# Optimization experiments

Measured on AMD Instinct MI355X. Metric: run time of the kernel, lower is better.

The kernel has to match this reference:

```python
import jax, jax.numpy as jnp
import numpy as np

K_SIZE = 7
D_MODEL = 128
D_Q = 64
N_HEADS = 4
D_FF = 512
EPS = 1e-5


def _windows(x, k):
    # x: [N,E,H,W] -> [N,E,P,H,W]; zero-padded local k x k windows,
    # row-major over (dy,dx), matching nn.Unfold ordering.
    p = k // 2
    N, E, H, W = x.shape
    xp = jnp.pad(x, ((0, 0), (0, 0), (p, p), (p, p)))
    ws = [xp[:, :, i:i + H, j:j + W] for i in range(k) for j in range(k)]
    return jnp.stack(ws, axis=2)


def _layernorm(x, g, b):
    m = jnp.mean(x, -1, keepdims=True)
    v = jnp.var(x, -1, keepdims=True)
    return (x - m) * jax.lax.rsqrt(v + EPS) * g + b


def setup_inputs() -> dict:
    key = jax.random.key(0)
    ks = jax.random.split(key, 12)
    E, Q, F = D_MODEL, D_Q, D_FF

    def g(k, shape, s=0.02):
        return jax.random.normal(k, shape, jnp.float32) * s

    return dict(
        x=jax.random.normal(ks[0], (4, E, 64, 64), jnp.float32),
        qcoeff=jax.random.normal(ks[1], (4, Q), jnp.float32),
        wq=g(ks[2], (E, E)), bq=jnp.zeros((E,), jnp.float32),
        wk=g(ks[3], (E, E)), bk=jnp.zeros((E,), jnp.float32),
        wv=g(ks[4], (E, E)), bv=jnp.zeros((E,), jnp.float32),
        rel_bias=jnp.zeros((N_HEADS, K_SIZE * K_SIZE), jnp.float32),
        ln1_g=jnp.ones((E,), jnp.float32), ln1_b=jnp.zeros((E,), jnp.float32),
        bil_w=g(ks[5], (E, E, Q)), bil_b=jnp.zeros((E,), jnp.float32),
        ln2_g=jnp.ones((E,), jnp.float32), ln2_b=jnp.zeros((E,), jnp.float32),
        w1=g(ks[6], (F, E)), b1=jnp.zeros((F,), jnp.float32),
        w2=g(ks[7], (E, F)), b2=jnp.zeros((E,), jnp.float32),
    )


def reference(x, qcoeff, wq, bq, wk, bk, wv, bv, rel_bias, ln1_g, ln1_b,
              bil_w, bil_b, ln2_g, ln2_b, w1, b1, w2, b2):
    N, E, H, W = x.shape
    Nh = N_HEADS
    Hd = E // Nh
    P = K_SIZE * K_SIZE

    x_nhwc = jnp.transpose(x, (0, 2, 3, 1))              # [N,H,W,E]
    xn = _layernorm(x_nhwc, ln1_g, ln1_b)
    xnc = jnp.transpose(xn, (0, 3, 1, 2))                # [N,E,H,W]

    # 1x1-conv projections
    q = jnp.einsum('nchw,oc->nohw', xnc, wq) + bq[None, :, None, None]
    k = jnp.einsum('nchw,oc->nohw', xnc, wk) + bk[None, :, None, None]
    v = jnp.einsum('nchw,oc->nohw', xnc, wv) + bv[None, :, None, None]

    # local windows of K/V: [N,Nh,Hd,P,H,W]
    Kw = _windows(k, K_SIZE).reshape(N, Nh, Hd, P, H, W)
    Vw = _windows(v, K_SIZE).reshape(N, Nh, Hd, P, H, W)
    Qh = q.reshape(N, Nh, Hd, H, W)

    scores = jnp.einsum('nhdyx,nhdpyx->nhpyx', Qh, Kw)
    scores = scores + rel_bias[None, :, :, None, None]
    attn = jax.nn.softmax(scores, axis=2)                # softmax over P
    out = jnp.einsum('nhpyx,nhdpyx->nhdyx', attn, Vw).reshape(N, E, H, W)
    z0 = jnp.transpose(out, (0, 2, 3, 1))                # [N,H,W,E]

    # Bilinear(z0, qcoeff): qcoeff constant per (H,W) -> contract once per batch
    t = jnp.einsum('oiq,nq->noi', bil_w, qcoeff)         # [N,E,E]
    z1 = jnp.einsum('nhwi,noi->nhwo', z0, t) + bil_b

    z2 = z1 + x_nhwc
    z3 = _layernorm(z2, ln2_g, ln2_b)
    h1 = jax.nn.gelu(z3 @ w1.T + b1, approximate=False)  # dropout inactive (eval)
    z4 = h1 @ w2.T + b2 + z2
    return jnp.transpose(z4, (0, 3, 1, 2))               # [N,E,H,W]
```

## Files before the change

### kernel.cpp

```cpp
#include <hip/hip_runtime.h>
#include <cmath>

#define EPS 1e-5f
#define SZ 2097152

typedef __attribute__((ext_vector_type(8))) short short8;
typedef __attribute__((ext_vector_type(4))) float floatx4;

__device__ __forceinline__ float dot4(float4 a, float4 b) {
  return fmaf(a.x, b.x, fmaf(a.y, b.y, fmaf(a.z, b.z, a.w * b.w)));
}

__device__ __forceinline__ short f2bf(float f) {
  union { float f; unsigned u; } v; v.f = f;
  unsigned r = v.u + 0x7fff + ((v.u >> 16) & 1);
  return (short)(r >> 16);
}

#define MFMA16(a, b, c) __builtin_amdgcn_mfma_f32_16x16x32_bf16(a, b, c, 0, 0, 0)

__global__ __launch_bounds__(256) void k_prep(const float* __restrict__ w1,
    const float* __restrict__ w2, const float* __restrict__ wq,
    const float* __restrict__ wk, const float* __restrict__ wv,
    const float* __restrict__ bil_w, const float* __restrict__ qcoeff,
    short* __restrict__ w1bf, short* __restrict__ w2bf,
    short* __restrict__ wqbf, short* __restrict__ wkbf, short* __restrict__ wvbf,
    short* __restrict__ tb) {
  __shared__ float qs[256];
  int tid = threadIdx.x;
  qs[tid] = qcoeff[tid];
  __syncthreads();
  int tid0 = blockIdx.x * 256 + tid;
  int stride = gridDim.x * 256;
  for (int i = tid0; i < 16384; i += stride) {
    int flat = i * 4; int f = flat >> 7, c = flat & 127;
    float4 v = *(const float4*)&w1[flat];
    short t4[4] = {f2bf(v.x), f2bf(v.y), f2bf(v.z), f2bf(v.w)};
    *(uint2*)&w1bf[f * 136 + c] = *(uint2*)t4;
  }
  for (int i = tid0; i < 16384; i += stride) {
    int flat = i * 4; int o = flat >> 9, j = flat & 511;
    int ck = j >> 7, jj = j & 127;
    float4 v = *(const float4*)&w2[flat];
    short t4[4] = {f2bf(v.x), f2bf(v.y), f2bf(v.z), f2bf(v.w)};
    *(uint2*)&w2bf[(ck * 128 + o) * 136 + jj] = *(uint2*)t4;
  }
  for (int i = tid0; i < 4096; i += stride) {
    int flat = i * 4; int o = flat >> 7, c = flat & 127;
    float4 a = *(const float4*)&wq[flat];
    float4 b = *(const float4*)&wk[flat];
    float4 cc = *(const float4*)&wv[flat];
    short ta[4] = {f2bf(a.x), f2bf(a.y), f2bf(a.z), f2bf(a.w)};
    short tb4[4] = {f2bf(b.x), f2bf(b.y), f2bf(b.z), f2bf(b.w)};
    short tc[4] = {f2bf(cc.x), f2bf(cc.y), f2bf(cc.z), f2bf(cc.w)};
    *(uint2*)&wqbf[o * 136 + c] = *(uint2*)ta;
    *(uint2*)&wkbf[o * 136 + c] = *(uint2*)tb4;
    *(uint2*)&wvbf[o * 136 + c] = *(uint2*)tc;
  }
  {
    int flat = tid0;
    const float* wrow = bil_w + (size_t)flat * 64;
    float acc[4] = {0.f, 0.f, 0.f, 0.f};
    for (int qq = 0; qq < 64; qq += 4) {
      float4 w4 = *(const float4*)&wrow[qq];
#pragma unroll
      for (int nn = 0; nn < 4; ++nn) {
        const float* qc = &qs[nn * 64 + qq];
        acc[nn] = fmaf(w4.x, qc[0], fmaf(w4.y, qc[1], fmaf(w4.z, qc[2], fmaf(w4.w, qc[3], acc[nn]))));
      }
    }
    int o = flat >> 7, i = flat & 127;
#pragma unroll
    for (int nn = 0; nn < 4; ++nn) tb[nn * 17408 + o * 136 + i] = f2bf(acc[nn]);
  }
}

__global__ __launch_bounds__(512) void k_qkvln(const float* __restrict__ x,
    const float* __restrict__ g, const float* __restrict__ b,
    const short* __restrict__ wqbf, const short* __restrict__ wkbf,
    const short* __restrict__ wvbf, const float* __restrict__ bq,
    const float* __restrict__ bk, const float* __restrict__ bv,
    float* __restrict__ xnhwc, short* __restrict__ qbf,
    short* __restrict__ kbf, short* __restrict__ vtb) {
  __shared__ float tile[128 * 33];
  __shared__ float mres[32], rres[32];
  __shared__ __align__(16) short xs[32 * 136];
  __shared__ __align__(16) short ws[128 * 136];
  int tid = threadIdx.x;
  int bid = blockIdx.x;
  int half = bid & 1, ny = bid >> 1;
  int n = ny >> 6, y = ny & 63;
  const float* xb = x + (size_t)n * 524288 + y * 64 + half * 32;
  for (int it = 0; it < 8; ++it) {
    int flat = it * 512 + tid;
    int c = flat >> 5, xpl = flat & 31;
    tile[c * 33 + xpl] = xb[(size_t)c * 4096 + xpl];
  }
  __syncthreads();
  {
    int pxl = tid >> 4, cl = tid & 15;
    float s = 0.f, sq = 0.f;
#pragma unroll
    for (int j = 0; j < 8; ++j) {
      float v = tile[(cl * 8 + j) * 33 + pxl];
      s += v; sq += v * v;
    }
    s += __shfl_xor(s, 1);  sq += __shfl_xor(sq, 1);
    s += __shfl_xor(s, 2);  sq += __shfl_xor(sq, 2);
    s += __shfl_xor(s, 4);  sq += __shfl_xor(sq, 4);
    s += __shfl_xor(s, 8);  sq += __shfl_xor(sq, 8);
    if (cl == 0) {
      float m = s * (1.f / 128.f);
      float var = sq * (1.f / 128.f) - m * m;
      mres[pxl] = m;
      rres[pxl] = rsqrtf(var + EPS);
    }
  }
  __syncthreads();
  size_t rowbase = (size_t)ny * 8192 + half * 4096;
  for (int it = 0; it < 8; ++it) {
    int flat = it * 512 + tid;
    int c = flat & 127, pxl = flat >> 7;
    float v = tile[c * 33 + pxl];
    xnhwc[rowbase + flat] = v;
    xs[pxl * 136 + c] = f2bf((v - mres[pxl]) * rres[pxl] * g[c] + b[c]);
  }
  __syncthreads();
  int w = tid >> 6, lane = tid & 63;
  int quad = lane >> 4, r16 = lane & 15;
  int wm = w & 1, wn = w >> 1;
  int stripl = wm * 16;
  short8 a[4];
#pragma unroll
  for (int kk = 0; kk < 4; ++kk)
    a[kk] = *(const short8*)&xs[(stripl + r16) * 136 + kk * 32 + quad * 8];
  const short* wptr[3] = {wqbf, wkbf, wvbf};
  const float* bptr[3] = {bq, bk, bv};
  for (int m = 0; m < 3; ++m) {
    __syncthreads();
    const short* wp = wptr[m];
    for (int i = tid; i < 2176; i += 512)
      *(short8*)&ws[i * 8] = *(const short8*)&wp[i * 8];
    __syncthreads();
    const float* bb = bptr[m];
#pragma unroll
    for (int nt = 0; nt < 2; ++nt) {
      int o0 = wn * 32 + nt * 16;
      floatx4 acc = {0.f, 0.f, 0.f, 0.f};
#pragma unroll
      for (int kk = 0; kk < 4; ++kk) {
        short8 bfr = *(const short8*)&ws[(o0 + r16) * 136 + kk * 32 + quad * 8];
        acc = MFMA16(a[kk], bfr, acc);
      }
      float bv2 = bb[o0 + r16];
      if (m < 2) {
        short* dst = (m == 0) ? qbf : kbf;
#pragma unroll
        for (int r = 0; r < 4; ++r) {
          int pxl = stripl + quad * 4 + r;
          dst[rowbase + pxl * 128 + o0 + r16] = f2bf(acc[r] + bv2);
        }
      } else {
        short t4[4] = {f2bf(acc[0] + bv2), f2bf(acc[1] + bv2),
                       f2bf(acc[2] + bv2), f2bf(acc[3] + bv2)};
        *(uint2*)&vtb[(size_t)(n * 128 + o0 + r16) * 4096 + y * 64 + half * 32 +
                      stripl + quad * 4] = *(uint2*)t4;
      }
    }
  }
}

__global__ __launch_bounds__(512, 4) void k_at(const short* __restrict__ qbf,
    const short* __restrict__ kbf, const short* __restrict__ vtb,
    const float* __restrict__ rel_bias, const short* __restrict__ tb,
    const float* __restrict__ bil_b, const float* __restrict__ xnhwc,
    const float* __restrict__ g2, const float* __restrict__ b2ln,
    const short* __restrict__ w1bf, const float* __restrict__ b1,
    const short* __restrict__ w2bf, const float* __restrict__ b2,
    float* __restrict__ out) {
  __shared__ __align__(16) char smem[70272];
  short* h1s = (short*)smem;
  short* z3s = (short*)(smem + 44672);
  float* z2s = (float*)(smem + 53376);
  int tid = threadIdx.x;
  int bid = blockIdx.x;
  int half = bid & 1, ny = bid >> 1;
  int n = ny >> 6, y = ny & 63;
  int w16 = tid >> 6, lane = tid & 63;
  int quad = lane >> 4, r16 = lane & 15;
  size_t rowbase = (size_t)ny * 8192;
  int wm = w16 & 1, wn = w16 >> 1;
  int stripL = wm * 16;
  float xres[2][4];
#pragma unroll
  for (int nt = 0; nt < 2; ++nt)
#pragma unroll
    for (int r = 0; r < 4; ++r)
      xres[nt][r] = xnhwc[rowbase + (half * 32 + stripL + quad * 4 + r) * 128 +
                          wn * 32 + nt * 16 + r16];
  {
    int h = w16 >> 1, swl = w16 & 1;
    int sg = half * 2 + swl;
    int strip = sg * 16;
    float* ssfw = (float*)(smem + w16 * 3200);
    short* Abw = (short*)(smem + 25600 + w16 * 2176);
    float* biasw = (float*)(smem + 43008 + w16 * 208);
    {
      unsigned* ad = (unsigned*)Abw;
      for (int i = lane; i < 544; i += 64) ad[i] = 0u;
    }
    if (lane < 49) biasw[lane] = rel_bias[h * 49 + lane];
    const short* qrow = qbf + (size_t)n * 524288 + (size_t)y * 8192 + h * 32;
    short8 qf = *(const short8*)&qrow[(strip + r16) * 128 + quad * 8];
    const short* kbp = kbf + (size_t)n * 524288 + h * 32;
#pragma unroll
    for (int r = 0; r < 7; ++r) {
      int yy = y + r - 3;
      bool yok = (unsigned)yy < 64u;
      int yyc = min(max(yy, 0), 63);
#pragma unroll
      for (int t = 0; t < 2; ++t) {
        int xxc = (sg + t) * 16 + r16;
        int gx = xxc - 3;
        bool ok = yok && ((unsigned)gx < 64u);
        int gxc = min(max(gx, 0), 63);
        short8 bf = *(const short8*)&kbp[(size_t)(yyc * 64 + gxc) * 128 + quad * 8];
        floatx4 c = MFMA16(qf, bf, ((floatx4){0.f, 0.f, 0.f, 0.f}));
#pragma unroll
        for (int rr = 0; rr < 4; ++rr) {
          int lrow = quad * 4 + rr;
          int dx = xxc - (strip + lrow);
          if ((unsigned)dx < 7u) {
            float val = ok ? c[rr] : 0.f;
            ssfw[lrow * 50 + r * 7 + dx] = val + biasw[r * 7 + dx];
          }
        }
      }
    }
    {
      int lrow = lane >> 2, sub = lane & 3;
      int p0 = sub * 12;
      float sv[13];
      float mx = -1e30f;
#pragma unroll
      for (int pi = 0; pi < 13; ++pi) {
        sv[pi] = ssfw[lrow * 50 + p0 + pi];
        mx = fmaxf(mx, sv[pi]);
      }
      mx = fmaxf(mx, __shfl_xor(mx, 1));
      mx = fmaxf(mx, __shfl_xor(mx, 2));
      float sum = 0.f;
#pragma unroll
      for (int pi = 0; pi < 13; ++pi) {
        float e = __expf(sv[pi] - mx);
        if (pi == 12 && sub != 3) e = 0.f;
        sv[pi] = e; sum += e;
      }
      sum += __shfl_xor(sum, 1);
      sum += __shfl_xor(sum, 2);
      float inv = 1.f / sum;
#pragma unroll
      for (int pi = 0; pi < 13; ++pi)
        if (pi < 12 || sub == 3) ssfw[lrow * 50 + p0 + pi] = sv[pi] * inv;
    }
    floatx4 oacc[2] = {(floatx4){0.f, 0.f, 0.f, 0.f}, (floatx4){0.f, 0.f, 0.f, 0.f}};
    int kk0 = (sg == 3) ? 1 : 0;
    int kk1 = (sg == 0) ? 0 : 1;
    int lrow = lane >> 2, sub = lane & 3;
    int pxg = strip + lrow;
    const short* vbp = vtb + (size_t)(n * 128 + h * 32) * 4096;
    for (int r = 0; r < 7; ++r) {
      int yy = y + r - 3;
      bool yok = (unsigned)yy < 64u;
      int yyc = min(max(yy, 0), 63);
      int c0 = pxg + sub - 3;
      if ((unsigned)c0 < 64u) Abw[lrow * 68 + c0] = f2bf(ssfw[lrow * 50 + r * 7 + sub]);
      int c1 = pxg + sub + 1;
      if (sub < 3 && (unsigned)c1 < 64u)
        Abw[lrow * 68 + c1] = f2bf(ssfw[lrow * 50 + r * 7 + sub + 4]);
      for (int kk = kk0; kk <= kk1; ++kk) {
        short8 af = *(const short8*)&Abw[r16 * 68 + kk * 32 + quad * 8];
#pragma unroll
        for (int nt = 0; nt < 2; ++nt) {
          short8 vf = *(const short8*)&vbp[(size_t)(nt * 16 + r16) * 4096 + yyc * 64 + kk * 32 + quad * 8];
          if (!yok) vf = (short8){0, 0, 0, 0, 0, 0, 0, 0};
          oacc[nt] = MFMA16(af, vf, oacc[nt]);
        }
      }
    }
#pragma unroll
    for (int nt = 0; nt < 2; ++nt)
#pragma unroll
      for (int rr = 0; rr < 4; ++rr) {
        int pxl = swl * 16 + quad * 4 + rr;
        z3s[pxl * 136 + h * 32 + nt * 16 + r16] = f2bf(oacc[nt][rr]);
      }
  }
  __syncthreads();
  {
    const short* tn = tb + (size_t)n * 17408;
    short8 a[4];
#pragma unroll
    for (int kk = 0; kk < 4; ++kk)
      a[kk] = *(const short8*)&z3s[(stripL + r16) * 136 + kk * 32 + quad * 8];
#pragma unroll
    for (int nt = 0; nt < 2; ++nt) {
      int o0 = wn * 32 + nt * 16;
      floatx4 acc = {0.f, 0.f, 0.f, 0.f};
#pragma unroll
      for (int kk = 0; kk < 4; ++kk) {
        short8 bfr = *(const short8*)&tn[(o0 + r16) * 136 + kk * 32 + quad * 8];
        acc = MFMA16(a[kk], bfr, acc);
      }
      float bb = bil_b[o0 + r16];
#pragma unroll
      for (int r = 0; r < 4; ++r) {
        int pxl = stripL + quad * 4 + r;
        z2s[pxl * 132 + o0 + r16] = acc[r] + bb + xres[nt][r];
      }
    }
  }
  __syncthreads();
  {
    int px = tid >> 4, cl = tid & 15;
    float4 v0 = *(const float4*)&z2s[px * 132 + cl * 8];
    float4 v1 = *(const float4*)&z2s[px * 132 + cl * 8 + 4];
    float s = v0.x + v0.y + v0.z + v0.w + v1.x + v1.y + v1.z + v1.w;
    float sq = dot4(v0, v0) + dot4(v1, v1);
    s += __shfl_xor(s, 1);  sq += __shfl_xor(sq, 1);
    s += __shfl_xor(s, 2);  sq += __shfl_xor(sq, 2);
    s += __shfl_xor(s, 4);  sq += __shfl_xor(sq, 4);
    s += __shfl_xor(s, 8);  sq += __shfl_xor(sq, 8);
    float m = s * (1.f / 128.f);
    float var = sq * (1.f / 128.f) - m * m;
    float rr = rsqrtf(var + EPS);
    int c0 = cl * 8;
    short t8[8];
#pragma unroll
    for (int j = 0; j < 8; ++j) {
      float vv = (j < 4) ? (&v0.x)[j] : (&v1.x)[j - 4];
      t8[j] = f2bf((vv - m) * rr * g2[c0 + j] + b2ln[c0 + j]);
    }
    *(uint4*)&z3s[px * 136 + c0] = *(uint4*)t8;
  }
  __syncthreads();
  short8 a3[4];
#pragma unroll
  for (int kk = 0; kk < 4; ++kk)
    a3[kk] = *(const short8*)&z3s[(stripL + r16) * 136 + kk * 32 + quad * 8];
  floatx4 zacc[2];
  zacc[0] = (floatx4){0.f, 0.f, 0.f, 0.f};
  zacc[1] = (floatx4){0.f, 0.f, 0.f, 0.f};
  for (int fc = 0; fc < 512; fc += 128) {
#pragma unroll
    for (int nt = 0; nt < 2; ++nt) {
      int f0 = wn * 32 + nt * 16;
      floatx4 acc = {0.f, 0.f, 0.f, 0.f};
#pragma unroll
      for (int kk = 0; kk < 4; ++kk) {
        short8 bfr = *(const short8*)&w1bf[(fc + f0 + r16) * 136 + kk * 32 + quad * 8];
        acc = MFMA16(a3[kk], bfr, acc);
      }
      float bb1 = b1[fc + f0 + r16];
#pragma unroll
      for (int r = 0; r < 4; ++r) {
        float hv = acc[r] + bb1;
        float ge = 0.5f * hv * (1.f + erff(hv * 0.70710678118f));
        h1s[(stripL + quad * 4 + r) * 136 + f0 + r16] = f2bf(ge);
      }
    }
    __syncthreads();
    short8 ah[4];
#pragma unroll
    for (int kk = 0; kk < 4; ++kk)
      ah[kk] = *(const short8*)&h1s[(stripL + r16) * 136 + kk * 32 + quad * 8];
    const short* w2src = w2bf + (fc >> 7) * 17408;
#pragma unroll
    for (int nt = 0; nt < 2; ++nt) {
      int o0 = wn * 32 + nt * 16;
#pragma unroll
      for (int kk = 0; kk < 4; ++kk) {
        short8 bfr = *(const short8*)&w2src[(o0 + r16) * 136 + kk * 32 + quad * 8];
        zacc[nt] = MFMA16(ah[kk], bfr, zacc[nt]);
      }
    }
    __syncthreads();
  }
#pragma unroll
  for (int nt = 0; nt < 2; ++nt) {
    int o = wn * 32 + nt * 16 + r16;
    float bb = b2[o];
    float res[4];
#pragma unroll
    for (int r = 0; r < 4; ++r)
      res[r] = zacc[nt][r] + bb + z2s[(stripL + quad * 4 + r) * 132 + o];
    *(float4*)&out[(((size_t)(n * 128 + o)) * 64 + y) * 64 + half * 32 + stripL + quad * 4] =
        *(float4*)res;
  }
}

extern "C" void kernel_launch(void* const* d_in, const int* in_sizes, int n_in,
                              void* d_out, int out_size, void* d_ws, size_t ws_size,
                              hipStream_t stream) {
  const float* x        = (const float*)d_in[0];
  const float* qcoeff   = (const float*)d_in[1];
  const float* wq       = (const float*)d_in[2];
  const float* bq       = (const float*)d_in[3];
  const float* wk       = (const float*)d_in[4];
  const float* bk       = (const float*)d_in[5];
  const float* wv       = (const float*)d_in[6];
  const float* bv       = (const float*)d_in[7];
  const float* rel_bias = (const float*)d_in[8];
  const float* ln1_g    = (const float*)d_in[9];
  const float* ln1_b    = (const float*)d_in[10];
  const float* bil_w    = (const float*)d_in[11];
  const float* bil_b    = (const float*)d_in[12];
  const float* ln2_g    = (const float*)d_in[13];
  const float* ln2_b    = (const float*)d_in[14];
  const float* w1       = (const float*)d_in[15];
  const float* b1       = (const float*)d_in[16];
  const float* w2       = (const float*)d_in[17];
  const float* b2       = (const float*)d_in[18];
  float* out = (float*)d_out;

  float* ws = (float*)d_ws;
  float* x_nhwc = ws;
  short* qbf = (short*)(ws + 2 * SZ);
  short* kbf = qbf + SZ;
  short* vtb = kbf + SZ;
  short* bf     = (short*)(ws + 4 * SZ);
  short* tb     = bf;
  short* w1bf   = bf + 4 * 17408;
  short* w2bf   = w1bf + 512 * 136;
  short* wqbf   = w2bf + 4 * 17408;
  short* wkbf   = wqbf + 17408;
  short* wvbf   = wkbf + 17408;

  k_prep<<<64, 256, 0, stream>>>(w1, w2, wq, wk, wv, bil_w, qcoeff,
                                 w1bf, w2bf, wqbf, wkbf, wvbf, tb);
  k_qkvln<<<512, 512, 0, stream>>>(x, ln1_g, ln1_b, wqbf, wkbf, wvbf,
                                   bq, bk, bv, x_nhwc, qbf, kbf, vtb);
  k_at<<<512, 512, 0, stream>>>(qbf, kbf, vtb, rel_bias, tb, bil_b, x_nhwc,
                                ln2_g, ln2_b, w1bf, b1, w2bf, b2, out);
}
```

Before: 153.9 us.

## Prefetch K/V/weight fragments into registers and widen prep grid

In the attention kernel, all K fragments for the 7x2 window tiles are loaded up front, and V rows are double-buffered so the next row's loads overlap the current row's MFMAs. Bilinear weights and W1/W2 fragments are also prefetched into registers ahead of use, so global-load latency is hidden behind compute. The prep kernel's bilinear contraction becomes a grid-stride loop and the prep launch grows to 256 blocks for more parallelism. The cost is much higher register pressure, which may lower occupancy or cause spills.

```diff
diff --git a/kernel.cpp b/kernel.cpp
--- a/kernel.cpp
+++ b/kernel.cpp
@@ -57,8 +57,7 @@
     *(uint2*)&wkbf[o * 136 + c] = *(uint2*)tb4;
     *(uint2*)&wvbf[o * 136 + c] = *(uint2*)tc;
   }
-  {
-    int flat = tid0;
+  for (int flat = tid0; flat < 16384; flat += stride) {
     const float* wrow = bil_w + (size_t)flat * 64;
     float acc[4] = {0.f, 0.f, 0.f, 0.f};
     for (int qq = 0; qq < 64; qq += 4) {
@@ -191,6 +190,7 @@
   size_t rowbase = (size_t)ny * 8192;
   int wm = w16 & 1, wn = w16 >> 1;
   int stripL = wm * 16;
+  const short* tn = tb + (size_t)n * 17408;
   float xres[2][4];
 #pragma unroll
   for (int nt = 0; nt < 2; ++nt)
@@ -198,6 +198,7 @@
     for (int r = 0; r < 4; ++r)
       xres[nt][r] = xnhwc[rowbase + (half * 32 + stripL + quad * 4 + r) * 128 +
                           wn * 32 + nt * 16 + r16];
+  short8 tf[2][4];
   {
     int h = w16 >> 1, swl = w16 & 1;
     int sg = half * 2 + swl;
@@ -205,27 +206,32 @@
     float* ssfw = (float*)(smem + w16 * 3200);
     short* Abw = (short*)(smem + 25600 + w16 * 2176);
     float* biasw = (float*)(smem + 43008 + w16 * 208);
+    const short* qrow = qbf + (size_t)n * 524288 + (size_t)y * 8192 + h * 32;
+    const short* kbp = kbf + (size_t)n * 524288 + h * 32;
+    short8 qf = *(const short8*)&qrow[(strip + r16) * 128 + quad * 8];
+    short8 kf[7][2];
+#pragma unroll
+    for (int r = 0; r < 7; ++r) {
+      int yyc = min(max(y + r - 3, 0), 63);
+#pragma unroll
+      for (int t = 0; t < 2; ++t) {
+        int gxc = min(max((sg + t) * 16 + r16 - 3, 0), 63);
+        kf[r][t] = *(const short8*)&kbp[(size_t)(yyc * 64 + gxc) * 128 + quad * 8];
+      }
+    }
     {
       unsigned* ad = (unsigned*)Abw;
       for (int i = lane; i < 544; i += 64) ad[i] = 0u;
     }
     if (lane < 49) biasw[lane] = rel_bias[h * 49 + lane];
-    const short* qrow = qbf + (size_t)n * 524288 + (size_t)y * 8192 + h * 32;
-    short8 qf = *(const short8*)&qrow[(strip + r16) * 128 + quad * 8];
-    const short* kbp = kbf + (size_t)n * 524288 + h * 32;
 #pragma unroll
     for (int r = 0; r < 7; ++r) {
-      int yy = y + r - 3;
-      bool yok = (unsigned)yy < 64u;
-      int yyc = min(max(yy, 0), 63);
+      bool yok = (unsigned)(y + r - 3) < 64u;
 #pragma unroll
       for (int t = 0; t < 2; ++t) {
         int xxc = (sg + t) * 16 + r16;
-        int gx = xxc - 3;
-        bool ok = yok && ((unsigned)gx < 64u);
-        int gxc = min(max(gx, 0), 63);
-        short8 bf = *(const short8*)&kbp[(size_t)(yyc * 64 + gxc) * 128 + quad * 8];
-        floatx4 c = MFMA16(qf, bf, ((floatx4){0.f, 0.f, 0.f, 0.f}));
+        bool ok = yok && ((unsigned)(xxc - 3) < 64u);
+        floatx4 c = MFMA16(qf, kf[r][t], ((floatx4){0.f, 0.f, 0.f, 0.f}));
 #pragma unroll
         for (int rr = 0; rr < 4; ++rr) {
           int lrow = quad * 4 + rr;
@@ -264,30 +270,48 @@
         if (pi < 12 || sub == 3) ssfw[lrow * 50 + p0 + pi] = sv[pi] * inv;
     }
     floatx4 oacc[2] = {(floatx4){0.f, 0.f, 0.f, 0.f}, (floatx4){0.f, 0.f, 0.f, 0.f}};
-    int kk0 = (sg == 3) ? 1 : 0;
-    int kk1 = (sg == 0) ? 0 : 1;
     int lrow = lane >> 2, sub = lane & 3;
     int pxg = strip + lrow;
     const short* vbp = vtb + (size_t)(n * 128 + h * 32) * 4096;
+    short8 vf[2][2][2];
+    {
+      int yyc0 = min(max(y - 3, 0), 63);
+#pragma unroll
+      for (int kk = 0; kk < 2; ++kk)
+#pragma unroll
+        for (int nt = 0; nt < 2; ++nt)
+          vf[0][kk][nt] = *(const short8*)&vbp[(size_t)(nt * 16 + r16) * 4096 + yyc0 * 64 + kk * 32 + quad * 8];
+    }
+#pragma unroll
     for (int r = 0; r < 7; ++r) {
-      int yy = y + r - 3;
-      bool yok = (unsigned)yy < 64u;
-      int yyc = min(max(yy, 0), 63);
+      if (r < 6) {
+        int yycn = min(max(y + r - 2, 0), 63);
+#pragma unroll
+        for (int kk = 0; kk < 2; ++kk)
+#pragma unroll
+          for (int nt = 0; nt < 2; ++nt)
+            vf[(r + 1) & 1][kk][nt] = *(const short8*)&vbp[(size_t)(nt * 16 + r16) * 4096 + yycn * 64 + kk * 32 + quad * 8];
+      }
       int c0 = pxg + sub - 3;
       if ((unsigned)c0 < 64u) Abw[lrow * 68 + c0] = f2bf(ssfw[lrow * 50 + r * 7 + sub]);
       int c1 = pxg + sub + 1;
       if (sub < 3 && (unsigned)c1 < 64u)
         Abw[lrow * 68 + c1] = f2bf(ssfw[lrow * 50 + r * 7 + sub + 4]);
-      for (int kk = kk0; kk <= kk1; ++kk) {
-        short8 af = *(const short8*)&Abw[r16 * 68 + kk * 32 + quad * 8];
-#pragma unroll
-        for (int nt = 0; nt < 2; ++nt) {
-          short8 vf = *(const short8*)&vbp[(size_t)(nt * 16 + r16) * 4096 + yyc * 64 + kk * 32 + quad * 8];
-          if (!yok) vf = (short8){0, 0, 0, 0, 0, 0, 0, 0};
-          oacc[nt] = MFMA16(af, vf, oacc[nt]);
+      if ((unsigned)(y + r - 3) < 64u) {
+#pragma unroll
+        for (int kk = 0; kk < 2; ++kk) {
+          short8 af = *(const short8*)&Abw[r16 * 68 + kk * 32 + quad * 8];
+#pragma unroll
+          for (int nt = 0; nt < 2; ++nt)
+            oacc[nt] = MFMA16(af, vf[r & 1][kk][nt], oacc[nt]);
         }
       }
     }
+#pragma unroll
+    for (int nt = 0; nt < 2; ++nt)
+#pragma unroll
+      for (int kk = 0; kk < 4; ++kk)
+        tf[nt][kk] = *(const short8*)&tn[(wn * 32 + nt * 16 + r16) * 136 + kk * 32 + quad * 8];
 #pragma unroll
     for (int nt = 0; nt < 2; ++nt)
 #pragma unroll
@@ -298,7 +322,6 @@
   }
   __syncthreads();
   {
-    const short* tn = tb + (size_t)n * 17408;
     short8 a[4];
 #pragma unroll
     for (int kk = 0; kk < 4; ++kk)
@@ -308,10 +331,8 @@
       int o0 = wn * 32 + nt * 16;
       floatx4 acc = {0.f, 0.f, 0.f, 0.f};
 #pragma unroll
-      for (int kk = 0; kk < 4; ++kk) {
-        short8 bfr = *(const short8*)&tn[(o0 + r16) * 136 + kk * 32 + quad * 8];
-        acc = MFMA16(a[kk], bfr, acc);
-      }
+      for (int kk = 0; kk < 4; ++kk)
+        acc = MFMA16(a[kk], tf[nt][kk], acc);
       float bb = bil_b[o0 + r16];
 #pragma unroll
       for (int r = 0; r < 4; ++r) {
@@ -321,6 +342,12 @@
     }
   }
   __syncthreads();
+  short8 wA[2][4];
+#pragma unroll
+  for (int nt = 0; nt < 2; ++nt)
+#pragma unroll
+    for (int kk = 0; kk < 4; ++kk)
+      wA[nt][kk] = *(const short8*)&w1bf[(wn * 32 + nt * 16 + r16) * 136 + kk * 32 + quad * 8];
   {
     int px = tid >> 4, cl = tid & 15;
     float4 v0 = *(const float4*)&z2s[px * 132 + cl * 8];
@@ -344,27 +371,44 @@
     *(uint4*)&z3s[px * 136 + c0] = *(uint4*)t8;
   }
   __syncthreads();
-  short8 a3[4];
-#pragma unroll
-  for (int kk = 0; kk < 4; ++kk)
-    a3[kk] = *(const short8*)&z3s[(stripL + r16) * 136 + kk * 32 + quad * 8];
   floatx4 zacc[2];
   zacc[0] = (floatx4){0.f, 0.f, 0.f, 0.f};
   zacc[1] = (floatx4){0.f, 0.f, 0.f, 0.f};
   for (int fc = 0; fc < 512; fc += 128) {
+    short8 wB[2][4];
+#pragma unroll
+    for (int nt = 0; nt < 2; ++nt)
+#pragma unroll
+      for (int kk = 0; kk < 4; ++kk)
+        wB[nt][kk] = *(const short8*)&w2bf[((fc >> 7) * 128 + wn * 32 + nt * 16 + r16) * 136 + kk * 32 + quad * 8];
+    float bb1v[2];
+    bb1v[0] = b1[fc + wn * 32 + r16];
+    bb1v[1] = b1[fc + wn * 32 + 16 + r16];
+    short8 a3[4];
+#pragma unroll
+    for (int kk = 0; kk < 4; ++kk)
+      a3[kk] = *(const short8*)&z3s[(stripL + r16) * 136 + kk * 32 + quad * 8];
+    floatx4 hacc[2];
+#pragma unroll
+    for (int nt = 0; nt < 2; ++nt) {
+      hacc[nt] = (floatx4){0.f, 0.f, 0.f, 0.f};
+#pragma unroll
+      for (int kk = 0; kk < 4; ++kk)
+        hacc[nt] = MFMA16(a3[kk], wA[nt][kk], hacc[nt]);
+    }
+    if (fc < 384) {
+#pragma unroll
+      for (int nt = 0; nt < 2; ++nt)
+#pragma unroll
+        for (int kk = 0; kk < 4; ++kk)
+          wA[nt][kk] = *(const short8*)&w1bf[(fc + 128 + wn * 32 + nt * 16 + r16) * 136 + kk * 32 + quad * 8];
+    }
 #pragma unroll
     for (int nt = 0; nt < 2; ++nt) {
       int f0 = wn * 32 + nt * 16;
-      floatx4 acc = {0.f, 0.f, 0.f, 0.f};
-#pragma unroll
-      for (int kk = 0; kk < 4; ++kk) {
-        short8 bfr = *(const short8*)&w1bf[(fc + f0 + r16) * 136 + kk * 32 + quad * 8];
-        acc = MFMA16(a3[kk], bfr, acc);
-      }
-      float bb1 = b1[fc + f0 + r16];
 #pragma unroll
       for (int r = 0; r < 4; ++r) {
-        float hv = acc[r] + bb1;
+        float hv = hacc[nt][r] + bb1v[nt];
         float ge = 0.5f * hv * (1.f + erff(hv * 0.70710678118f));
         h1s[(stripL + quad * 4 + r) * 136 + f0 + r16] = f2bf(ge);
       }
@@ -374,16 +418,11 @@
 #pragma unroll
     for (int kk = 0; kk < 4; ++kk)
       ah[kk] = *(const short8*)&h1s[(stripL + r16) * 136 + kk * 32 + quad * 8];
-    const short* w2src = w2bf + (fc >> 7) * 17408;
-#pragma unroll
-    for (int nt = 0; nt < 2; ++nt) {
-      int o0 = wn * 32 + nt * 16;
-#pragma unroll
-      for (int kk = 0; kk < 4; ++kk) {
-        short8 bfr = *(const short8*)&w2src[(o0 + r16) * 136 + kk * 32 + quad * 8];
-        zacc[nt] = MFMA16(ah[kk], bfr, zacc[nt]);
-      }
-    }
+#pragma unroll
+    for (int nt = 0; nt < 2; ++nt)
+#pragma unroll
+      for (int kk = 0; kk < 4; ++kk)
+        zacc[nt] = MFMA16(ah[kk], wB[nt][kk], zacc[nt]);
     __syncthreads();
   }
 #pragma unroll
@@ -436,8 +475,8 @@
   short* wkbf   = wqbf + 17408;
   short* wvbf   = wkbf + 17408;
 
-  k_prep<<<64, 256, 0, stream>>>(w1, w2, wq, wk, wv, bil_w, qcoeff,
-                                 w1bf, w2bf, wqbf, wkbf, wvbf, tb);
+  k_prep<<<256, 256, 0, stream>>>(w1, w2, wq, wk, wv, bil_w, qcoeff,
+                                  w1bf, w2bf, wqbf, wkbf, wvbf, tb);
   k_qkvln<<<512, 512, 0, stream>>>(x, ln1_g, ln1_b, wqbf, wkbf, wvbf,
                                    bq, bk, bv, x_nhwc, qbf, kbf, vtb);
   k_at<<<512, 512, 0, stream>>>(qbf, kbf, vtb, rel_bias, tb, bil_b, x_nhwc,
```

After: 151.0 us. No clear change (-1.9%).
